# Kernel optimization log

Hardware: AMD Instinct MI355X
Metric: run time of the kernel (lower is better)

## Reference

```python
import jax, jax.numpy as jnp
import numpy as np

S = 8      # n_subspaces
K = 256    # n_codewords
D = 64     # d_codeword
EPS = 1e-5


def setup_inputs() -> dict:
    key = jax.random.key(0)
    k1, k2 = jax.random.split(key)
    z = jax.random.normal(k1, (8, 4096, S * D), dtype=jnp.float32)
    # learned codebook, matches nn.Parameter(torch.randn([S, K, D]))
    weight = jax.random.normal(k2, (S, K, D), dtype=jnp.float32)
    return {"z": z, "weight": weight}


def reference(z, weight):
    # mode='train', method='k-means'
    zf = z.reshape(-1, S, D).transpose(1, 0, 2)  # [S, N, D]
    x2 = jnp.sum(zf * zf, axis=-1, keepdims=True)        # [S, N, 1]
    c2 = jnp.sum(weight * weight, axis=-1)[:, None, :]   # [S, 1, K]
    xc = jnp.einsum('snd,skd->snk', zf, weight)          # [S, N, K]
    dist = jnp.sqrt(jnp.maximum(x2 + c2 - 2.0 * xc, 0.0))
    idx = jnp.argmin(dist, axis=-1)                      # [S, N]
    # codebook gather: weight[s, idx[s, n], :]
    zq_flat = jnp.take_along_axis(weight, idx[:, :, None], axis=1)  # [S, N, D]
    z_q = zq_flat.transpose(1, 0, 2).reshape(z.shape)
    # k-means soft-assignment loss
    dist_c = jnp.maximum(dist, EPS)
    attn = jax.nn.softmax(-jnp.log(dist_c), axis=-1)     # [S, N, K]
    z_w = jnp.einsum('snk,skd->snd', attn, weight)       # [S, N, D]
    loss_w = jnp.mean((z_w - zq_flat) ** 2)
    loss_q = jnp.mean((zf - zq_flat) ** 2)
    loss = loss_w + loss_q
    # straight-through estimator
    z_q_st = z + jax.lax.stop_gradient(z_q - z)
    return z_q_st, loss
```

## Files before the change

### kernel.cpp

```cpp
#include <hip/hip_runtime.h>
#include <math.h>


#define SNS   8
#define KCW   256
#define DCW   64
#define NPTS  32768
#define SD    512
#define PT    64
#define EPS2F 1e-10f

#define W_STRIDE 68
#define Z_STRIDE 68
#define R_STRIDE 264

#define W_OFF   0
#define W_FL    (KCW * W_STRIDE)
#define Z_OFF   (W_OFF + W_FL)
#define Z_FL    (PT * Z_STRIDE)
#define R_OFF   (Z_OFF + Z_FL)
#define R_FL    (8 * 8 * R_STRIDE)
#define C2_OFF  (R_OFF + R_FL)
#define X2_OFF  (C2_OFF + KCW)
#define RED_OFF (X2_OFF + PT)
#define LDS_FL  (RED_OFF + 8)
#define LDS_BYTES (LDS_FL * 4)

__global__ void pq_zero_loss(float* loss) { *loss = 0.0f; }

__global__ __launch_bounds__(512, 2)
void pq_main(const float* __restrict__ z, const float* __restrict__ w,
             float* __restrict__ out, float* __restrict__ loss_out) {
  extern __shared__ float lds[];
  float* w68 = lds + W_OFF;
  float* zl  = lds + Z_OFF;
  float* rt  = lds + R_OFF;
  float* c2l = lds + C2_OFF;
  float* x2l = lds + X2_OFF;
  float* red = lds + RED_OFF;

  const int t    = threadIdx.x;
  const int s    = blockIdx.x >> 9;
  const int tile = blockIdx.x & 511;
  const int n0   = tile * PT;

  {
    const float* ws = w + (size_t)s * (KCW * DCW);
    #pragma unroll
    for (int pass = 0; pass < 8; ++pass) {
      int idx = pass * 512 + t;
      int k  = idx >> 4;
      int d4 = idx & 15;
      float4 v = *(const float4*)(ws + idx * 4);
      *(float4*)(w68 + k * W_STRIDE + d4 * 4) = v;
    }
  }
  {
    #pragma unroll
    for (int pass = 0; pass < 2; ++pass) {
      int idx = pass * 512 + t;
      int i  = idx >> 4;
      int d4 = idx & 15;
      float4 v = *(const float4*)(z + (size_t)(n0 + i) * SD + s * DCW + d4 * 4);
      *(float4*)(zl + i * Z_STRIDE + d4 * 4) = v;
      float sq = v.x*v.x + v.y*v.y + v.z*v.z + v.w*v.w;
      sq += __shfl_xor(sq, 1);
      sq += __shfl_xor(sq, 2);
      sq += __shfl_xor(sq, 4);
      sq += __shfl_xor(sq, 8);
      if (d4 == 0) x2l[i] = sq;
    }
  }
  __syncthreads();
  if (t < KCW) {
    float acc = 0.f;
    const float* row = w68 + t * W_STRIDE;
    #pragma unroll
    for (int d4 = 0; d4 < 16; ++d4) {
      float4 v = *(const float4*)(row + d4 * 4);
      acc += v.x*v.x + v.y*v.y + v.z*v.z + v.w*v.w;
    }
    c2l[t] = acc;
  }
  __syncthreads();

  const int wave = t >> 6;
  const int l    = t & 63;
  const int p0   = wave * 8;
  float* rtw = rt + wave * (8 * R_STRIDE);

  float c2r[4];
  #pragma unroll
  for (int g = 0; g < 4; ++g) c2r[g] = c2l[l + 64 * g];

  float acc[8][4];
  #pragma unroll
  for (int p = 0; p < 8; ++p)
    #pragma unroll
    for (int g = 0; g < 4; ++g) acc[p][g] = 0.f;

  {
    const float* wbase = w68 + l * W_STRIDE;
    #pragma unroll 4
    for (int d4 = 0; d4 < 16; ++d4) {
      float4 wv[4];
      #pragma unroll
      for (int g = 0; g < 4; ++g)
        wv[g] = *(const float4*)(wbase + g * (64 * W_STRIDE) + d4 * 4);
      #pragma unroll
      for (int p = 0; p < 8; ++p) {
        const float4 zv = *(const float4*)(zl + (p0 + p) * Z_STRIDE + d4 * 4);
        #pragma unroll
        for (int g = 0; g < 4; ++g) {
          acc[p][g] = fmaf(zv.x, wv[g].x, acc[p][g]);
          acc[p][g] = fmaf(zv.y, wv[g].y, acc[p][g]);
          acc[p][g] = fmaf(zv.z, wv[g].z, acc[p][g]);
          acc[p][g] = fmaf(zv.w, wv[g].w, acc[p][g]);
        }
      }
    }
  }

  float dmin[8]; int kmin[8]; float rsum[8];
  #pragma unroll
  for (int p = 0; p < 8; ++p) {
    const float x2 = x2l[p0 + p];
    float d2g[4];
    #pragma unroll
    for (int g = 0; g < 4; ++g) {
      float m = fmaf(-2.f, acc[p][g], x2 + c2r[g]);
      d2g[g] = fmaxf(m, 0.f);
    }
    float dm = d2g[0];
    int   km = l;
    float rs = 0.f;
    #pragma unroll
    for (int g = 0; g < 4; ++g) {
      float r = rsqrtf(fmaxf(d2g[g], EPS2F));
      rs += r;
      rtw[p * R_STRIDE + l + 64 * g] = r;
      if (g > 0 && d2g[g] < dm) { dm = d2g[g]; km = l + 64 * g; }
    }
    dmin[p] = dm; kmin[p] = km; rsum[p] = rs;
  }
  #pragma unroll
  for (int off = 1; off < 64; off <<= 1) {
    #pragma unroll
    for (int p = 0; p < 8; ++p) {
      float od = __shfl_xor(dmin[p], off);
      int   ok = __shfl_xor(kmin[p], off);
      float oR = __shfl_xor(rsum[p], off);
      if (od < dmin[p] || (od == dmin[p] && ok < kmin[p])) { dmin[p] = od; kmin[p] = ok; }
      rsum[p] += oR;
    }
  }

  float lq_lane = 0.f;
  #pragma unroll
  for (int p = 0; p < 8; ++p) {
    const float wq = w68[kmin[p] * W_STRIDE + l];
    const int n = n0 + p0 + p;
    out[(size_t)n * SD + s * DCW + l] = wq;
    float dq = zl[(p0 + p) * Z_STRIDE + l] - wq;
    lq_lane = fmaf(dq, dq, lq_lane);
  }
  __syncthreads();

  const int d4b = l & 15;
  const int kk  = l >> 4;
  float u[8][4];
  #pragma unroll
  for (int p = 0; p < 8; ++p)
    #pragma unroll
    for (int c = 0; c < 4; ++c) u[p][c] = 0.f;

  {
    const float* wB = w68 + d4b * 4;
    #pragma unroll 2
    for (int step = 0; step < 16; ++step) {
      const int se = (step + 2 * kk) & 15;
      const int k0 = kk * 64 + 4 * se;
      float4 r4[8];
      #pragma unroll
      for (int p = 0; p < 8; ++p)
        r4[p] = *(const float4*)(rtw + p * R_STRIDE + k0);
      #pragma unroll
      for (int j = 0; j < 4; ++j) {
        const float4 wv = *(const float4*)(wB + (k0 + j) * W_STRIDE);
        #pragma unroll
        for (int p = 0; p < 8; ++p) {
          const float rj = (j == 0) ? r4[p].x : (j == 1) ? r4[p].y
                         : (j == 2) ? r4[p].z : r4[p].w;
          u[p][0] = fmaf(rj, wv.x, u[p][0]);
          u[p][1] = fmaf(rj, wv.y, u[p][1]);
          u[p][2] = fmaf(rj, wv.z, u[p][2]);
          u[p][3] = fmaf(rj, wv.w, u[p][3]);
        }
      }
    }
  }
  #pragma unroll
  for (int p = 0; p < 8; ++p)
    #pragma unroll
    for (int c = 0; c < 4; ++c) {
      float v = u[p][c];
      v += __shfl_xor(v, 16);
      v += __shfl_xor(v, 32);
      u[p][c] = v;
    }

  float lw_lane = 0.f;
  #pragma unroll
  for (int p = 0; p < 8; ++p) {
    const float invR = 1.0f / rsum[p];
    const float4 zq = *(const float4*)(w68 + kmin[p] * W_STRIDE + d4b * 4);
    float ex = fmaf(u[p][0], invR, -zq.x);
    float ey = fmaf(u[p][1], invR, -zq.y);
    float ez = fmaf(u[p][2], invR, -zq.z);
    float ew = fmaf(u[p][3], invR, -zq.w);
    lw_lane += ex*ex + ey*ey + ez*ez + ew*ew;
  }

  float total = lq_lane + 0.25f * lw_lane;
  #pragma unroll
  for (int off = 1; off < 64; off <<= 1) total += __shfl_xor(total, off);
  if (l == 0) red[wave] = total;
  __syncthreads();
  if (t == 0) {
    float sum = 0.f;
    #pragma unroll
    for (int wv = 0; wv < 8; ++wv) sum += red[wv];
    atomicAdd(loss_out, sum * (1.0f / 16777216.0f));
  }
}

extern "C" void kernel_launch(void* const* d_in, const int* in_sizes, int n_in,
                              void* d_out, int out_size, void* d_ws, size_t ws_size,
                              hipStream_t stream) {
  const float* z = (const float*)d_in[0];
  const float* w = (const float*)d_in[1];
  float* out  = (float*)d_out;
  float* loss = out + (size_t)NPTS * SD;

  (void)hipFuncSetAttribute(reinterpret_cast<const void*>(pq_main),
                            hipFuncAttributeMaxDynamicSharedMemorySize, LDS_BYTES);

  pq_zero_loss<<<1, 1, 0, stream>>>(loss);
  pq_main<<<dim3((NPTS / PT) * SNS), dim3(512), LDS_BYTES, stream>>>(z, w, out, loss);
}
```

Measured before the change: 465.1 us.

## Move distance and soft-assignment matmuls to bf16x3 split MFMA

Replaces the FP32 FMA loops for both the z·W distance GEMM and the attn·W weighted sum with MFMA bf16 instructions. To keep near-FP32 accuracy, inputs are split into high/mid/low bf16 parts, with six MFMA products for distances and two for the second GEMM. LDS layouts are XOR-swizzled, and the argmin/rsum reduction becomes a cross-wave two-stage reduction. The codebook is re-read from global memory and transposed into LDS. The costs are more LDS (about 150KB, which may limit occupancy to one block per CU), extra syncs, and a risk of argmin ties flipping or loss drifting from bf16 attention weights.

```diff
diff --git a/kernel.cpp b/kernel.cpp
--- a/kernel.cpp
+++ b/kernel.cpp
@@ -2,234 +2,320 @@
 #include <math.h>
 
 
-#define SNS   8
-#define KCW   256
-#define DCW   64
-#define NPTS  32768
-#define SD    512
-#define PT    64
-#define EPS2F 1e-10f
-
-#define W_STRIDE 68
-#define Z_STRIDE 68
-#define R_STRIDE 264
-
-#define W_OFF   0
-#define W_FL    (KCW * W_STRIDE)
-#define Z_OFF   (W_OFF + W_FL)
-#define Z_FL    (PT * Z_STRIDE)
-#define R_OFF   (Z_OFF + Z_FL)
-#define R_FL    (8 * 8 * R_STRIDE)
-#define C2_OFF  (R_OFF + R_FL)
-#define X2_OFF  (C2_OFF + KCW)
-#define RED_OFF (X2_OFF + PT)
-#define LDS_FL  (RED_OFF + 8)
-#define LDS_BYTES (LDS_FL * 4)
+typedef __attribute__((ext_vector_type(8))) short b16x8;
+typedef __attribute__((ext_vector_type(4))) float f32x4;
+typedef __attribute__((ext_vector_type(4))) int i32x4;
+typedef __attribute__((ext_vector_type(4))) unsigned short u16x4;
+
+#define SNS 8
+#define KCW 256
+#define DCW 64
+#define NPTS 32768
+#define SD 512
+#define PT 64
+
+#define WH    0
+#define WM    32768
+#define WL    65536
+#define ZP0   98304
+#define RPL   98304
+#define C2O   131072
+#define X2O   132096
+#define PMINO 132352
+#define PKIDO 133376
+#define PRSUMO 134400
+#define INVRO 135424
+#define KMINO 135680
+#define REDO  135936
+#define ZQFO  136192
+#define LDS_BYTES 153600
+
+__device__ __forceinline__ unsigned short f2bf(float x) {
+  unsigned u = __float_as_uint(x);
+  return (unsigned short)((u + 0x7FFFu + ((u >> 16) & 1u)) >> 16);
+}
+__device__ __forceinline__ float bf2f(unsigned short b) {
+  return __uint_as_float(((unsigned)b) << 16);
+}
 
 __global__ void pq_zero_loss(float* loss) { *loss = 0.0f; }
 
 __global__ __launch_bounds__(512, 2)
 void pq_main(const float* __restrict__ z, const float* __restrict__ w,
              float* __restrict__ out, float* __restrict__ loss_out) {
-  extern __shared__ float lds[];
-  float* w68 = lds + W_OFF;
-  float* zl  = lds + Z_OFF;
-  float* rt  = lds + R_OFF;
-  float* c2l = lds + C2_OFF;
-  float* x2l = lds + X2_OFF;
-  float* red = lds + RED_OFF;
-
-  const int t    = threadIdx.x;
-  const int s    = blockIdx.x >> 9;
-  const int tile = blockIdx.x & 511;
-  const int n0   = tile * PT;
+  extern __shared__ char lds[];
+  const int t  = threadIdx.x;
+  const int s  = blockIdx.x >> 9;
+  const int n0 = (blockIdx.x & 511) * PT;
+  const int wv = t >> 6;
+  const int l  = t & 63;
+  const int g  = l >> 4;
+  const int fr = l & 15;
+
+  float* c2l = (float*)(lds + C2O);
+  float* x2l = (float*)(lds + X2O);
 
   {
     const float* ws = w + (size_t)s * (KCW * DCW);
     #pragma unroll
     for (int pass = 0; pass < 8; ++pass) {
-      int idx = pass * 512 + t;
-      int k  = idx >> 4;
-      int d4 = idx & 15;
-      float4 v = *(const float4*)(ws + idx * 4);
-      *(float4*)(w68 + k * W_STRIDE + d4 * 4) = v;
-    }
-  }
-  {
+      int fidx = pass * 512 + t;
+      int k = fidx >> 4, d4 = fidx & 15;
+      float4 v = *(const float4*)(ws + fidx * 4);
+      u16x4 hq, mq, lq;
+      float xs[4] = {v.x, v.y, v.z, v.w};
+      #pragma unroll
+      for (int j = 0; j < 4; ++j) {
+        unsigned short h = f2bf(xs[j]); float hf = bf2f(h);
+        unsigned short m = f2bf(xs[j] - hf); float mf = bf2f(m);
+        unsigned short o = f2bf((xs[j] - hf) - mf);
+        hq[j] = h; mq[j] = m; lq[j] = o;
+      }
+      int addr = k * 128 + (((d4 >> 1) ^ (k & 7)) << 4) + (d4 & 1) * 8;
+      *(u16x4*)(lds + WH + addr) = hq;
+      *(u16x4*)(lds + WM + addr) = mq;
+      *(u16x4*)(lds + WL + addr) = lq;
+      float sq = v.x*v.x + v.y*v.y + v.z*v.z + v.w*v.w;
+      sq += __shfl_xor(sq, 1); sq += __shfl_xor(sq, 2);
+      sq += __shfl_xor(sq, 4); sq += __shfl_xor(sq, 8);
+      if (d4 == 0) c2l[k] = sq;
+    }
     #pragma unroll
     for (int pass = 0; pass < 2; ++pass) {
       int idx = pass * 512 + t;
-      int i  = idx >> 4;
-      int d4 = idx & 15;
+      int i = idx >> 4, d4 = idx & 15;
       float4 v = *(const float4*)(z + (size_t)(n0 + i) * SD + s * DCW + d4 * 4);
-      *(float4*)(zl + i * Z_STRIDE + d4 * 4) = v;
+      u16x4 hq, mq, lq;
+      float xs[4] = {v.x, v.y, v.z, v.w};
+      #pragma unroll
+      for (int j = 0; j < 4; ++j) {
+        unsigned short h = f2bf(xs[j]); float hf = bf2f(h);
+        unsigned short m = f2bf(xs[j] - hf); float mf = bf2f(m);
+        unsigned short o = f2bf((xs[j] - hf) - mf);
+        hq[j] = h; mq[j] = m; lq[j] = o;
+      }
+      int addr = i * 128 + (((d4 >> 1) ^ (i & 7)) << 4) + (d4 & 1) * 8;
+      *(u16x4*)(lds + ZP0 + 0     + addr) = hq;
+      *(u16x4*)(lds + ZP0 + 8192  + addr) = mq;
+      *(u16x4*)(lds + ZP0 + 16384 + addr) = lq;
       float sq = v.x*v.x + v.y*v.y + v.z*v.z + v.w*v.w;
-      sq += __shfl_xor(sq, 1);
-      sq += __shfl_xor(sq, 2);
-      sq += __shfl_xor(sq, 4);
-      sq += __shfl_xor(sq, 8);
+      sq += __shfl_xor(sq, 1); sq += __shfl_xor(sq, 2);
+      sq += __shfl_xor(sq, 4); sq += __shfl_xor(sq, 8);
       if (d4 == 0) x2l[i] = sq;
     }
   }
   __syncthreads();
-  if (t < KCW) {
-    float acc = 0.f;
-    const float* row = w68 + t * W_STRIDE;
-    #pragma unroll
-    for (int d4 = 0; d4 < 16; ++d4) {
-      float4 v = *(const float4*)(row + d4 * 4);
-      acc += v.x*v.x + v.y*v.y + v.z*v.z + v.w*v.w;
-    }
-    c2l[t] = acc;
-  }
-  __syncthreads();
-
-  const int wave = t >> 6;
-  const int l    = t & 63;
-  const int p0   = wave * 8;
-  float* rtw = rt + wave * (8 * R_STRIDE);
-
-  float c2r[4];
-  #pragma unroll
-  for (int g = 0; g < 4; ++g) c2r[g] = c2l[l + 64 * g];
-
-  float acc[8][4];
-  #pragma unroll
-  for (int p = 0; p < 8; ++p)
-    #pragma unroll
-    for (int g = 0; g < 4; ++g) acc[p][g] = 0.f;
-
-  {
-    const float* wbase = w68 + l * W_STRIDE;
-    #pragma unroll 4
-    for (int d4 = 0; d4 < 16; ++d4) {
-      float4 wv[4];
-      #pragma unroll
-      for (int g = 0; g < 4; ++g)
-        wv[g] = *(const float4*)(wbase + g * (64 * W_STRIDE) + d4 * 4);
-      #pragma unroll
-      for (int p = 0; p < 8; ++p) {
-        const float4 zv = *(const float4*)(zl + (p0 + p) * Z_STRIDE + d4 * 4);
+
+  const int mb = wv >> 2;
+  const int nb = wv & 3;
+  b16x8 za[3][2][2];
+  #pragma unroll
+  for (int pl = 0; pl < 3; ++pl)
+    #pragma unroll
+    for (int mt2 = 0; mt2 < 2; ++mt2)
+      #pragma unroll
+      for (int ks = 0; ks < 2; ++ks) {
+        int row = mb * 32 + mt2 * 16 + fr;
+        int addr = ZP0 + pl * 8192 + row * 128 + ((((4*ks + g) ^ (row & 7))) << 4);
+        za[pl][mt2][ks] = *(const b16x8*)(lds + addr);
+      }
+  f32x4 acc[2][4];
+  #pragma unroll
+  for (int m2 = 0; m2 < 2; ++m2)
+    #pragma unroll
+    for (int nt = 0; nt < 4; ++nt)
+      #pragma unroll
+      for (int c = 0; c < 4; ++c) acc[m2][nt][c] = 0.f;
+
+  #pragma unroll
+  for (int ntp = 0; ntp < 2; ++ntp) {
+    #pragma unroll
+    for (int ks = 0; ks < 2; ++ks) {
+      b16x8 bh[2], bm[2], bl[2];
+      #pragma unroll
+      for (int e = 0; e < 2; ++e) {
+        int krow = nb * 64 + (2*ntp + e) * 16 + fr;
+        int ab = krow * 128 + ((((4*ks + g) ^ (krow & 7))) << 4);
+        bh[e] = *(const b16x8*)(lds + WH + ab);
+        bm[e] = *(const b16x8*)(lds + WM + ab);
+        bl[e] = *(const b16x8*)(lds + WL + ab);
+      }
+      #pragma unroll
+      for (int e = 0; e < 2; ++e)
         #pragma unroll
-        for (int g = 0; g < 4; ++g) {
-          acc[p][g] = fmaf(zv.x, wv[g].x, acc[p][g]);
-          acc[p][g] = fmaf(zv.y, wv[g].y, acc[p][g]);
-          acc[p][g] = fmaf(zv.z, wv[g].z, acc[p][g]);
-          acc[p][g] = fmaf(zv.w, wv[g].w, acc[p][g]);
+        for (int m2 = 0; m2 < 2; ++m2) {
+          int nt = 2*ntp + e;
+          f32x4 a = acc[m2][nt];
+          a = __builtin_amdgcn_mfma_f32_16x16x32_bf16(za[0][m2][ks], bh[e], a, 0, 0, 0);
+          a = __builtin_amdgcn_mfma_f32_16x16x32_bf16(za[0][m2][ks], bm[e], a, 0, 0, 0);
+          a = __builtin_amdgcn_mfma_f32_16x16x32_bf16(za[1][m2][ks], bh[e], a, 0, 0, 0);
+          a = __builtin_amdgcn_mfma_f32_16x16x32_bf16(za[0][m2][ks], bl[e], a, 0, 0, 0);
+          a = __builtin_amdgcn_mfma_f32_16x16x32_bf16(za[2][m2][ks], bh[e], a, 0, 0, 0);
+          a = __builtin_amdgcn_mfma_f32_16x16x32_bf16(za[1][m2][ks], bm[e], a, 0, 0, 0);
+          acc[m2][nt] = a;
         }
-      }
-    }
-  }
-
-  float dmin[8]; int kmin[8]; float rsum[8];
-  #pragma unroll
-  for (int p = 0; p < 8; ++p) {
-    const float x2 = x2l[p0 + p];
-    float d2g[4];
-    #pragma unroll
-    for (int g = 0; g < 4; ++g) {
-      float m = fmaf(-2.f, acc[p][g], x2 + c2r[g]);
-      d2g[g] = fmaxf(m, 0.f);
-    }
-    float dm = d2g[0];
-    int   km = l;
-    float rs = 0.f;
-    #pragma unroll
-    for (int g = 0; g < 4; ++g) {
-      float r = rsqrtf(fmaxf(d2g[g], EPS2F));
-      rs += r;
-      rtw[p * R_STRIDE + l + 64 * g] = r;
-      if (g > 0 && d2g[g] < dm) { dm = d2g[g]; km = l + 64 * g; }
-    }
-    dmin[p] = dm; kmin[p] = km; rsum[p] = rs;
-  }
-  #pragma unroll
-  for (int off = 1; off < 64; off <<= 1) {
-    #pragma unroll
-    for (int p = 0; p < 8; ++p) {
-      float od = __shfl_xor(dmin[p], off);
-      int   ok = __shfl_xor(kmin[p], off);
-      float oR = __shfl_xor(rsum[p], off);
-      if (od < dmin[p] || (od == dmin[p] && ok < kmin[p])) { dmin[p] = od; kmin[p] = ok; }
-      rsum[p] += oR;
-    }
-  }
-
-  float lq_lane = 0.f;
-  #pragma unroll
-  for (int p = 0; p < 8; ++p) {
-    const float wq = w68[kmin[p] * W_STRIDE + l];
-    const int n = n0 + p0 + p;
-    out[(size_t)n * SD + s * DCW + l] = wq;
-    float dq = zl[(p0 + p) * Z_STRIDE + l] - wq;
-    lq_lane = fmaf(dq, dq, lq_lane);
-  }
-  __syncthreads();
-
-  const int d4b = l & 15;
-  const int kk  = l >> 4;
-  float u[8][4];
-  #pragma unroll
-  for (int p = 0; p < 8; ++p)
-    #pragma unroll
-    for (int c = 0; c < 4; ++c) u[p][c] = 0.f;
-
-  {
-    const float* wB = w68 + d4b * 4;
-    #pragma unroll 2
-    for (int step = 0; step < 16; ++step) {
-      const int se = (step + 2 * kk) & 15;
-      const int k0 = kk * 64 + 4 * se;
-      float4 r4[8];
-      #pragma unroll
-      for (int p = 0; p < 8; ++p)
-        r4[p] = *(const float4*)(rtw + p * R_STRIDE + k0);
+    }
+  }
+  __syncthreads();
+
+  {
+    float c2k[4];
+    #pragma unroll
+    for (int nt = 0; nt < 4; ++nt) c2k[nt] = c2l[nb * 64 + nt * 16 + fr];
+    float dm[8]; int km[8]; float rs[8];
+    #pragma unroll
+    for (int m2 = 0; m2 < 2; ++m2)
+      #pragma unroll
+      for (int i = 0; i < 4; ++i) {
+        int p = mb * 32 + m2 * 16 + g * 4 + i;
+        float x2p = x2l[p];
+        float bd = 3.4e38f; int bk = 0; float rsum = 0.f;
+        #pragma unroll
+        for (int nt = 0; nt < 4; ++nt) {
+          int k = nb * 64 + nt * 16 + fr;
+          float d2 = fmaxf(fmaf(-2.f, acc[m2][nt][i], x2p + c2k[nt]), 0.f);
+          float rv = rsqrtf(fmaxf(d2, 1e-10f));
+          rsum += rv;
+          int slot = (k >> 3) ^ (p & 7);
+          *(unsigned short*)(lds + RPL + p * 512 + (slot << 4) + (k & 7) * 2) = f2bf(rv);
+          if (d2 < bd) { bd = d2; bk = k; }
+        }
+        int q = m2 * 4 + i;
+        dm[q] = bd; km[q] = bk; rs[q] = rsum;
+      }
+    #pragma unroll
+    for (int off = 1; off < 16; off <<= 1) {
+      #pragma unroll
+      for (int q = 0; q < 8; ++q) {
+        float od = __shfl_xor(dm[q], off);
+        int   ok = __shfl_xor(km[q], off);
+        float orr = __shfl_xor(rs[q], off);
+        if (od < dm[q] || (od == dm[q] && ok < km[q])) { dm[q] = od; km[q] = ok; }
+        rs[q] += orr;
+      }
+    }
+    if (fr == 0) {
+      #pragma unroll
+      for (int q = 0; q < 8; ++q) {
+        int p = mb * 32 + (q >> 2) * 16 + g * 4 + (q & 3);
+        ((float*)(lds + PMINO))[p * 4 + nb] = dm[q];
+        ((int*)  (lds + PKIDO))[p * 4 + nb] = km[q];
+        ((float*)(lds + PRSUMO))[p * 4 + nb] = rs[q];
+      }
+    }
+  }
+  __syncthreads();
+
+  float lq_acc = 0.f;
+  if (t < 64) {
+    f32x4 pm = *(const f32x4*)(lds + PMINO + t * 16);
+    i32x4 pk = *(const i32x4*)(lds + PKIDO + t * 16);
+    f32x4 pr = *(const f32x4*)(lds + PRSUMO + t * 16);
+    float bd = pm[0]; int bk = pk[0];
+    #pragma unroll
+    for (int j = 1; j < 4; ++j) {
+      if (pm[j] < bd || (pm[j] == bd && pk[j] < bk)) { bd = pm[j]; bk = pk[j]; }
+    }
+    float rsum = (pr[0] + pr[1]) + (pr[2] + pr[3]);
+    ((int*)(lds + KMINO))[t] = bk;
+    ((float*)(lds + INVRO))[t] = 1.0f / rsum;
+    lq_acc = bd;
+  }
+  __syncthreads();
+
+  {
+    int p = t >> 3, d8 = t & 7;
+    int kmn = ((const int*)(lds + KMINO))[p];
+    int base = kmn * 128 + ((d8 ^ (kmn & 7)) << 4);
+    b16x8 hv = *(const b16x8*)(lds + WH + base);
+    b16x8 mv = *(const b16x8*)(lds + WM + base);
+    b16x8 lv = *(const b16x8*)(lds + WL + base);
+    f32x4 o0, o1;
+    #pragma unroll
+    for (int j = 0; j < 4; ++j) {
+      o0[j] = bf2f((unsigned short)hv[j]) + (bf2f((unsigned short)mv[j]) + bf2f((unsigned short)lv[j]));
+      o1[j] = bf2f((unsigned short)hv[j+4]) + (bf2f((unsigned short)mv[j+4]) + bf2f((unsigned short)lv[j+4]));
+    }
+    float* og = out + (size_t)(n0 + p) * SD + s * DCW + d8 * 8;
+    *(f32x4*)(og) = o0; *(f32x4*)(og + 4) = o1;
+    *(f32x4*)(lds + ZQFO + (p * 68 + d8 * 8) * 4) = o0;
+    *(f32x4*)(lds + ZQFO + (p * 68 + d8 * 8) * 4 + 16) = o1;
+  }
+  __syncthreads();
+
+  {
+    const float* ws = w + (size_t)s * (KCW * DCW);
+    #pragma unroll
+    for (int pass = 0; pass < 8; ++pass) {
+      int fidx = pass * 512 + t;
+      int k = fidx >> 4, d4 = fidx & 15;
+      float4 v = *(const float4*)(ws + fidx * 4);
+      float xs[4] = {v.x, v.y, v.z, v.w};
       #pragma unroll
       for (int j = 0; j < 4; ++j) {
-        const float4 wv = *(const float4*)(wB + (k0 + j) * W_STRIDE);
-        #pragma unroll
-        for (int p = 0; p < 8; ++p) {
-          const float rj = (j == 0) ? r4[p].x : (j == 1) ? r4[p].y
-                         : (j == 2) ? r4[p].z : r4[p].w;
-          u[p][0] = fmaf(rj, wv.x, u[p][0]);
-          u[p][1] = fmaf(rj, wv.y, u[p][1]);
-          u[p][2] = fmaf(rj, wv.z, u[p][2]);
-          u[p][3] = fmaf(rj, wv.w, u[p][3]);
-        }
-      }
-    }
-  }
-  #pragma unroll
-  for (int p = 0; p < 8; ++p)
-    #pragma unroll
-    for (int c = 0; c < 4; ++c) {
-      float v = u[p][c];
-      v += __shfl_xor(v, 16);
-      v += __shfl_xor(v, 32);
-      u[p][c] = v;
-    }
-
-  float lw_lane = 0.f;
-  #pragma unroll
-  for (int p = 0; p < 8; ++p) {
-    const float invR = 1.0f / rsum[p];
-    const float4 zq = *(const float4*)(w68 + kmin[p] * W_STRIDE + d4b * 4);
-    float ex = fmaf(u[p][0], invR, -zq.x);
-    float ey = fmaf(u[p][1], invR, -zq.y);
-    float ez = fmaf(u[p][2], invR, -zq.z);
-    float ew = fmaf(u[p][3], invR, -zq.w);
-    lw_lane += ex*ex + ey*ey + ez*ez + ew*ew;
-  }
-
-  float total = lq_lane + 0.25f * lw_lane;
+        int d = d4 * 4 + j;
+        unsigned short h = f2bf(xs[j]);
+        unsigned short m = f2bf(xs[j] - bf2f(h));
+        int addr = d * 512 + ((((k >> 3) ^ (d & 7))) << 4) + (k & 7) * 2;
+        *(unsigned short*)(lds + WH + addr) = h;
+        *(unsigned short*)(lds + WM + addr) = m;
+      }
+    }
+  }
+  __syncthreads();
+
+  const int mt  = wv >> 1;
+  const int np2 = wv & 1;
+  f32x4 bacc[2];
+  #pragma unroll
+  for (int n2 = 0; n2 < 2; ++n2)
+    #pragma unroll
+    for (int c = 0; c < 4; ++c) bacc[n2][c] = 0.f;
+  {
+    int arow = mt * 16 + fr;
+    #pragma unroll
+    for (int ks = 0; ks < 8; ++ks) {
+      int slot = ks * 4 + g;
+      b16x8 ra = *(const b16x8*)(lds + RPL + arow * 512 + ((slot ^ (arow & 7)) << 4));
+      #pragma unroll
+      for (int n2 = 0; n2 < 2; ++n2) {
+        int drow = (np2 * 2 + n2) * 16 + fr;
+        int ab = drow * 512 + ((slot ^ (drow & 7)) << 4);
+        b16x8 th = *(const b16x8*)(lds + WH + ab);
+        b16x8 tm = *(const b16x8*)(lds + WM + ab);
+        bacc[n2] = __builtin_amdgcn_mfma_f32_16x16x32_bf16(ra, th, bacc[n2], 0, 0, 0);
+        bacc[n2] = __builtin_amdgcn_mfma_f32_16x16x32_bf16(ra, tm, bacc[n2], 0, 0, 0);
+      }
+    }
+  }
+
+  float lw_acc = 0.f;
+  {
+    float iv[4];
+    #pragma unroll
+    for (int i = 0; i < 4; ++i)
+      iv[i] = ((const float*)(lds + INVRO))[mt * 16 + g * 4 + i];
+    #pragma unroll
+    for (int n2 = 0; n2 < 2; ++n2)
+      #pragma unroll
+      for (int i = 0; i < 4; ++i) {
+        int p = mt * 16 + g * 4 + i;
+        int d = (np2 * 2 + n2) * 16 + fr;
+        float zq = ((const float*)(lds + ZQFO))[p * 68 + d];
+        float e = fmaf(bacc[n2][i], iv[i], -zq);
+        lw_acc = fmaf(e, e, lw_acc);
+      }
+  }
+
+  float total = lq_acc + lw_acc;
   #pragma unroll
   for (int off = 1; off < 64; off <<= 1) total += __shfl_xor(total, off);
-  if (l == 0) red[wave] = total;
+  if (l == 0) ((float*)(lds + REDO))[wv] = total;
   __syncthreads();
   if (t == 0) {
     float sum = 0.f;
     #pragma unroll
-    for (int wv = 0; wv < 8; ++wv) sum += red[wv];
+    for (int i = 0; i < 8; ++i) sum += ((const float*)(lds + REDO))[i];
     atomicAdd(loss_out, sum * (1.0f / 16777216.0f));
   }
 }
```

New measurement: 378.9 us. -18.5%, faster.
